# Kernel optimization log

Hardware: AMD Instinct MI355X
Metric: run time of the kernel (lower is better)

Reference implementation:

```python
import jax, jax.numpy as jnp
import numpy as np

B, L, D = 4, 1024, 512
H, DK = 8, 64
NL = 4
M_REL = 7
NEG = jnp.float32(-2**32 + 1)


def _layernorm(x, g, b, eps=1e-5):
    mu = jnp.mean(x, axis=-1, keepdims=True)
    var = jnp.var(x, axis=-1, keepdims=True)
    return (x - mu) * jax.lax.rsqrt(var + eps) * g + b


def setup_inputs() -> dict:
    key = jax.random.key(0)
    ks = jax.random.split(key, 24)
    s = 0.02
    inp = {
        "x": jax.random.normal(ks[0], (B, L, D), jnp.float32),
        "maskPAD": jnp.ones((B, L, L), jnp.int32),
        "WQ": jax.random.normal(ks[1], (NL, D, H * DK), jnp.float32) * s,
        "bQ": jnp.zeros((NL, H * DK), jnp.float32),
        "WK": jax.random.normal(ks[2], (NL, D, H * DK), jnp.float32) * s,
        "bK": jnp.zeros((NL, H * DK), jnp.float32),
        "WV": jax.random.normal(ks[3], (NL, D, H * DK), jnp.float32) * s,
        "bV": jnp.zeros((NL, H * DK), jnp.float32),
        "WO": jax.random.normal(ks[4], (NL, H * DK, D), jnp.float32) * s,
        "bO": jnp.zeros((NL, D), jnp.float32),
        "embK": jax.random.normal(ks[5], (NL, 2 * M_REL + 1, H), jnp.float32) * s + 1.0,
        "embB": jax.random.normal(ks[6], (NL, 2 * M_REL + 1, H), jnp.float32) * s,
        "ln1_g": jnp.ones((NL, D), jnp.float32),
        "ln1_b": jnp.zeros((NL, D), jnp.float32),
        "ln2_g": jnp.ones((NL, D), jnp.float32),
        "ln2_b": jnp.zeros((NL, D), jnp.float32),
        "Wf1": jax.random.normal(ks[7], (NL, D, 4 * D), jnp.float32) * s,
        "bf1": jnp.zeros((NL, 4 * D), jnp.float32),
        "Wf2": jax.random.normal(ks[8], (NL, 4 * D, D), jnp.float32) * s,
        "bf2": jnp.zeros((NL, D), jnp.float32),
    }
    return inp


def _rel_idx():
    # posIdx is None -> arange-based relative distance with log-bucketing beyond M_REL
    pos = jnp.arange(L, dtype=jnp.float32)
    d = jnp.abs(pos[:, None] - pos[None, :])  # [L, L]
    d = jnp.where(d > M_REL, M_REL + jnp.log2(jnp.maximum(d - M_REL, 1.0)), d)
    return jnp.clip(d, 0, 2 * M_REL).astype(jnp.int32)  # [L, L]


def reference(x, maskPAD, WQ, bQ, WK, bK, WV, bV, WO, bO, embK, embB,
              ln1_g, ln1_b, ln2_g, ln2_b, Wf1, bf1, Wf2, bf2):
    idx = _rel_idx()  # [L, L]
    mask0 = (maskPAD == 0)[:, None, :, :]  # [B, 1, L, L]
    scale = 1.0 / np.sqrt(DK)

    qx = kx = vx = x
    pre = None
    for i in range(NL):
        q = (qx @ WQ[i] + bQ[i]).reshape(B, L, H, DK).transpose(0, 2, 1, 3)
        k = (kx @ WK[i] + bK[i]).reshape(B, L, H, DK).transpose(0, 2, 1, 3)
        v = (vx @ WV[i] + bV[i]).reshape(B, L, H, DK).transpose(0, 2, 1, 3)
        scores = jnp.einsum('bhqd,bhkd->bhqk', q, k) * scale  # [B,H,L,L]
        # multiplicative + additive relative-position bias
        kb = embK[i][idx].transpose(2, 0, 1)  # [H, L, L]
        bb = embB[i][idx].transpose(2, 0, 1)
        scores = scores * kb[None] + bb[None]
        if pre is not None:
            scores = scores + pre  # Realformer residual score carry
        scores = jnp.where(mask0, NEG, scores)
        alpha = jax.nn.softmax(scores, axis=-1)
        z = jnp.einsum('bhqk,bhkd->bhqd', alpha, v)
        z = z.transpose(0, 2, 1, 3).reshape(B, L, H * DK) @ WO[i] + bO[i]
        # FFN (Realformer: residual around vx)
        h = _layernorm(vx + z, ln1_g[i], ln1_b[i])
        ffn = jax.nn.gelu(h @ Wf1[i] + bf1[i], approximate=False) @ Wf2[i] + bf2[i]
        xo = _layernorm(h + ffn, ln2_g[i], ln2_b[i])
        qx = kx = vx = xo
        pre = scores
    return xo
```

## Files before the change

### kernel.cpp

```cpp
#include <hip/hip_runtime.h>
#include <stdint.h>

typedef unsigned short u16;
typedef short bf16x8_t __attribute__((ext_vector_type(8)));
typedef float f32x4_t __attribute__((ext_vector_type(4)));
typedef u16 u16x8_t __attribute__((ext_vector_type(8)));

#define MFMA16(a,b,c) __builtin_amdgcn_mfma_f32_16x16x32_bf16((a),(b),(c),0,0,0)

__device__ __forceinline__ u16 f2bf(float f) {
  uint32_t u = __float_as_uint(f);
  u += 0x7fffu + ((u >> 16) & 1u);
  return (u16)(u >> 16);
}
__device__ __forceinline__ float bf2f(u16 h) {
  return __uint_as_float(((uint32_t)h) << 16);
}
__device__ __forceinline__ void gload16(const void* g, void* l) {
  __builtin_amdgcn_global_load_lds(
      (__attribute__((address_space(1))) void*)const_cast<void*>(g),
      (__attribute__((address_space(3))) void*)l, 16, 0, 0);
}

__global__ __launch_bounds__(256) void cvt_bf16(const float* __restrict__ in,
                                                u16* __restrict__ out, int n4) {
  int i = blockIdx.x * 256 + threadIdx.x;
  if (i >= n4) return;
  float4 v = ((const float4*)in)[i];
  ushort4 o;
  o.x = f2bf(v.x); o.y = f2bf(v.y); o.z = f2bf(v.z); o.w = f2bf(v.w);
  ((ushort4*)out)[i] = o;
}

__global__ __launch_bounds__(256) void mask2plane(const int* __restrict__ mask,
                                                  u16* __restrict__ mp, int n8) {
  int i = blockIdx.x * 256 + threadIdx.x;
  if (i >= n8) return;
  int4 a = ((const int4*)mask)[i * 2], b = ((const int4*)mask)[i * 2 + 1];
  u16x8_t o;
  o[0] = a.x == 0 ? 0xCF80 : 0; o[1] = a.y == 0 ? 0xCF80 : 0;
  o[2] = a.z == 0 ? 0xCF80 : 0; o[3] = a.w == 0 ? 0xCF80 : 0;
  o[4] = b.x == 0 ? 0xCF80 : 0; o[5] = b.y == 0 ? 0xCF80 : 0;
  o[6] = b.z == 0 ? 0xCF80 : 0; o[7] = b.w == 0 ? 0xCF80 : 0;
  ((u16x8_t*)mp)[i] = o;
}

__global__ __launch_bounds__(256) void transpose_w(
    const float* __restrict__ in, u16* __restrict__ out, int K, int N,
    size_t in_bstride, size_t out_bstride, size_t out_off) {
  __shared__ float tile[32][33];
  int p = blockIdx.z;
  const float* ip = in + (size_t)p * in_bstride;
  u16* op = out + (size_t)p * out_bstride + out_off;
  int n0 = blockIdx.x * 32, k0 = blockIdx.y * 32;
  int tx = threadIdx.x & 31, ty = threadIdx.x >> 5;
#pragma unroll
  for (int r = 0; r < 4; r++) {
    int k = ty + r * 8;
    tile[k][tx] = ip[(size_t)(k0 + k) * N + n0 + tx];
  }
  __syncthreads();
#pragma unroll
  for (int r = 0; r < 4; r++) {
    int n = ty + r * 8;
    op[(size_t)(n0 + n) * K + k0 + tx] = f2bf(tile[tx][n]);
  }
}

__global__ __launch_bounds__(256) void ln_kernel(
    const float* __restrict__ in, const float* __restrict__ g,
    const float* __restrict__ bb, float* __restrict__ outf,
    u16* __restrict__ outb) {
  int row = blockIdx.x * 4 + (threadIdx.x >> 6);
  int lane = threadIdx.x & 63;
  const float4* ip = (const float4*)(in + (size_t)row * 512);
  float4 a = ip[lane * 2], c = ip[lane * 2 + 1];
  float s = a.x + a.y + a.z + a.w + c.x + c.y + c.z + c.w;
  float q = a.x * a.x + a.y * a.y + a.z * a.z + a.w * a.w +
            c.x * c.x + c.y * c.y + c.z * c.z + c.w * c.w;
#pragma unroll
  for (int m = 1; m < 64; m <<= 1) {
    s += __shfl_xor(s, m);
    q += __shfl_xor(q, m);
  }
  float mean = s * (1.0f / 512.0f);
  float var = q * (1.0f / 512.0f) - mean * mean;
  float rstd = rsqrtf(var + 1e-5f);
  const float4* gp = (const float4*)g;
  const float4* bp = (const float4*)bb;
  float4 g1 = gp[lane * 2], g2 = gp[lane * 2 + 1];
  float4 b1 = bp[lane * 2], b2 = bp[lane * 2 + 1];
  float4 y1, y2;
  y1.x = (a.x - mean) * rstd * g1.x + b1.x;
  y1.y = (a.y - mean) * rstd * g1.y + b1.y;
  y1.z = (a.z - mean) * rstd * g1.z + b1.z;
  y1.w = (a.w - mean) * rstd * g1.w + b1.w;
  y2.x = (c.x - mean) * rstd * g2.x + b2.x;
  y2.y = (c.y - mean) * rstd * g2.y + b2.y;
  y2.z = (c.z - mean) * rstd * g2.z + b2.z;
  y2.w = (c.w - mean) * rstd * g2.w + b2.w;
  ((float4*)(outf + (size_t)row * 512))[lane * 2] = y1;
  ((float4*)(outf + (size_t)row * 512))[lane * 2 + 1] = y2;
  ushort4 u1, u2;
  u1.x = f2bf(y1.x); u1.y = f2bf(y1.y); u1.z = f2bf(y1.z); u1.w = f2bf(y1.w);
  u2.x = f2bf(y2.x); u2.y = f2bf(y2.y); u2.z = f2bf(y2.z); u2.w = f2bf(y2.w);
  ((ushort4*)(outb + (size_t)row * 512))[lane * 2] = u1;
  ((ushort4*)(outb + (size_t)row * 512))[lane * 2 + 1] = u2;
}

template <int BM, int BN, int EPI>
__global__ __launch_bounds__(256) void gemmT(
    const u16* __restrict__ A, const u16* __restrict__ Bt, int K, int N,
    const float* __restrict__ f0, const float* __restrict__ f1,
    const float* __restrict__ f2, u16* __restrict__ o0, u16* __restrict__ o1,
    u16* __restrict__ o2, float* __restrict__ of) {
  constexpr int MFR = BM / 32, NFR = BN / 32;
  __shared__ u16 As[BM * 64];
  __shared__ u16 Bs[BN * 64];
  int t = threadIdx.x, lane = t & 63, w = t >> 6;
  int wr = w >> 1, wc = w & 1, lg = lane >> 4, li = lane & 15;
  int bn = blockIdx.x, bm = blockIdx.y;
  const u16* Ab = A + (size_t)bm * BM * K;
  const u16* Bb = Bt + (size_t)bn * BN * K;
  f32x4_t acc[MFR][NFR] = {};
  for (int k0 = 0; k0 < K; k0 += 64) {
    if (k0) __syncthreads();
#pragma unroll
    for (int i = 0; i < BM / 32; i++) {
      int o = i * 256 + t, r = o >> 3, c = o & 7, cs = c ^ (r & 7);
      gload16(Ab + (size_t)r * K + k0 + cs * 8, As + (i * 256 + (t & ~63)) * 8);
    }
#pragma unroll
    for (int i = 0; i < BN / 32; i++) {
      int o = i * 256 + t, r = o >> 3, c = o & 7, cs = c ^ (r & 7);
      gload16(Bb + (size_t)r * K + k0 + cs * 8, Bs + (i * 256 + (t & ~63)) * 8);
    }
    __syncthreads();
#pragma unroll
    for (int kk = 0; kk < 2; kk++) {
      bf16x8_t af[MFR], bfv[NFR];
#pragma unroll
      for (int m = 0; m < MFR; m++) {
        int r = wr * (BM / 2) + m * 16 + li;
        int cb = (kk * 4 + lg) ^ (r & 7);
        af[m] = *(const bf16x8_t*)(As + r * 64 + cb * 8);
      }
#pragma unroll
      for (int n = 0; n < NFR; n++) {
        int r = wc * (BN / 2) + n * 16 + li;
        int cb = (kk * 4 + lg) ^ (r & 7);
        bfv[n] = *(const bf16x8_t*)(Bs + r * 64 + cb * 8);
      }
#pragma unroll
      for (int m = 0; m < MFR; m++)
#pragma unroll
        for (int n = 0; n < NFR; n++)
          acc[m][n] = MFMA16(af[m], bfv[n], acc[m][n]);
    }
  }
#pragma unroll
  for (int m = 0; m < MFR; m++) {
#pragma unroll
    for (int n = 0; n < NFR; n++) {
      int col = bn * BN + wc * (BN / 2) + n * 16 + li;
#pragma unroll
      for (int j = 0; j < 4; j++) {
        int row = bm * BM + wr * (BM / 2) + m * 16 + lg * 4 + j;
        float v = acc[m][n][j];
        if constexpr (EPI == 0) {
          int which = col >> 9, hd = col & 511, hh = hd >> 6, dk = hd & 63;
          const float* bp = which == 0 ? f0 : (which == 1 ? f1 : f2);
          float val = v + bp[hd];
          int b2 = row >> 10, l = row & 1023;
          if (which == 0)
            o0[(((size_t)(b2 * 8 + hh)) * 1024 + l) * 64 + dk] = f2bf(val);
          else if (which == 1)
            o1[(((size_t)(b2 * 8 + hh)) * 1024 + l) * 64 + dk] = f2bf(val);
          else
            o2[(((size_t)(b2 * 8 + hh)) * 64 + dk) * 1024 + l] = f2bf(val);
        } else if constexpr (EPI == 1 || EPI == 3) {
          float val = v + f0[col] + f1[(size_t)row * 512 + col];
          of[(size_t)row * N + col] = val;
        } else {
          float x = v + f0[col];
          float val = 0.5f * x * (1.0f + erff(x * 0.70710678118f));
          o0[(size_t)row * N + col] = f2bf(val);
        }
      }
    }
  }
}

template <int WPRE>
__global__ __launch_bounds__(512, 4) void attn_kernel(
    const u16* __restrict__ qb, const u16* __restrict__ kb,
    const u16* __restrict__ vb, u16* __restrict__ zout,
    const u16* __restrict__ preR, u16* __restrict__ preW, int firstLayer,
    const float* __restrict__ embK, const float* __restrict__ embB) {
  __shared__ u16 Ks[2][64 * 64];
  __shared__ u16 Vs[2][64 * 64];
  __shared__ u16 Pre[8][16 * 64];
  __shared__ float2 lutKB[1024];
  int t = threadIdx.x, lane = t & 63, w = t >> 6;
  int half = w >> 2, wl = w & 3, lg = lane >> 4, li = lane & 15;
  int tl = t & 255;
  int bh = blockIdx.y, b = bh >> 3, h = bh & 7;
  int q0 = blockIdx.x * 64;
  for (int d = t; d < 1024; d += 512) {
    int idx = (d <= 7) ? d : min(14, 38 - __clz(d - 7));
    lutKB[d] = make_float2(embK[idx * 8 + h] * 0.125f, embB[idx * 8 + h]);
  }
  float fK = embK[14 * 8 + h] * 0.125f, fB = embB[14 * 8 + h];
  const u16* qrow = qb + ((size_t)bh * 1024 + q0 + wl * 16 + li) * 64;
  bf16x8_t qf[2];
  qf[0] = *(const bf16x8_t*)(qrow + lg * 8);
  qf[1] = *(const bf16x8_t*)(qrow + 32 + lg * 8);
  float lrow[4] = {0.f, 0.f, 0.f, 0.f};
  f32x4_t oacc[4] = {};
  const u16* kbase = kb + (size_t)bh * 65536;
  const u16* vbase = vb + (size_t)bh * 65536;
  const u16* prb = firstLayer ? preR + (size_t)b * 1048576
                              : preR + (size_t)bh * 1048576;
  u16* pwb = preW + (size_t)bh * 1048576;
  u16* prw = (u16*)Pre[w];
  int qrow0 = q0 + wl * 16;
  for (int kt = 0; kt < 8; ++kt) {
    if (kt) __syncthreads();
    int k0 = half * 512 + kt * 64;
#pragma unroll
    for (int i = 0; i < 2; i++) {
      int o = i * 256 + tl, r = o >> 3, c = o & 7, cs = c ^ (r & 7);
      gload16(kbase + (size_t)(k0 + r) * 64 + cs * 8,
              Ks[half] + (i * 256 + (tl & ~63)) * 8);
      gload16(vbase + (size_t)r * 1024 + k0 + cs * 8,
              Vs[half] + (i * 256 + (tl & ~63)) * 8);
    }
#pragma unroll
    for (int i = 0; i < 2; i++) {
      int g = i * 64 + lane, r = g >> 3, c = g & 7, cs = c ^ (r & 7);
      gload16(prb + (size_t)(qrow0 + r) * 1024 + k0 + cs * 8, prw + g * 8);
    }
    __syncthreads();
    f32x4_t s[4] = {};
    __builtin_amdgcn_s_setprio(1);
#pragma unroll
    for (int kk = 0; kk < 2; kk++) {
#pragma unroll
      for (int n = 0; n < 4; n++) {
        int r = n * 16 + li;
        int cb = (kk * 4 + lg) ^ (r & 7);
        bf16x8_t kf = *(const bf16x8_t*)(Ks[half] + r * 64 + cb * 8);
        s[n] = MFMA16(qf[kk], kf, s[n]);
      }
    }
    __builtin_amdgcn_s_setprio(0);
    float sv[4][4];
    bool farTile = (k0 - (qrow0 + 15) >= 135) || (qrow0 - (k0 + 63) >= 135);
    if (farTile) {
#pragma unroll
      for (int n = 0; n < 4; n++) {
#pragma unroll
        for (int j = 0; j < 4; j++) {
          int row = lg * 4 + j, col = n * 16 + li;
          int pidx = (row * 64 + col) ^ ((row & 7) << 3);
          float val = fmaf(s[n][j], fK, fB) + bf2f(prw[pidx]);
          prw[pidx] = f2bf(val);
          sv[n][j] = val;
        }
      }
    } else {
      int dbase = qrow0 + lg * 4 - k0 - li;
#pragma unroll
      for (int n = 0; n < 4; n++) {
#pragma unroll
        for (int j = 0; j < 4; j++) {
          int d = abs(dbase + j - n * 16);
          int row = lg * 4 + j, col = n * 16 + li;
          int pidx = (row * 64 + col) ^ ((row & 7) << 3);
          float2 kb2 = lutKB[d];
          float val = fmaf(s[n][j], kb2.x, kb2.y) + bf2f(prw[pidx]);
          prw[pidx] = f2bf(val);
          sv[n][j] = val;
        }
      }
    }
    if (WPRE) {
#pragma unroll
      for (int i = 0; i < 2; i++) {
        int g = i * 64 + lane, r = g >> 3, c = g & 7, cs = c ^ (r & 7);
        *(u16x8_t*)(pwb + (size_t)(qrow0 + r) * 1024 + k0 + cs * 8) =
            *(const u16x8_t*)(prw + g * 8);
      }
    }
#pragma unroll
    for (int n = 0; n < 4; n++) {
#pragma unroll
      for (int j = 0; j < 4; j++) {
        float p = __expf(sv[n][j]);
        lrow[j] += p;
        int row = lg * 4 + j, col = n * 16 + li;
        prw[(row * 64 + col) ^ ((row & 7) << 3)] = f2bf(p);
      }
    }
    __builtin_amdgcn_s_setprio(1);
#pragma unroll
    for (int kk = 0; kk < 2; kk++) {
      int cbp = (kk * 4 + lg) ^ (li & 7);
      bf16x8_t pf = *(const bf16x8_t*)(prw + li * 64 + cbp * 8);
#pragma unroll
      for (int n = 0; n < 4; n++) {
        int r = n * 16 + li;
        int cb = (kk * 4 + lg) ^ (r & 7);
        bf16x8_t vf = *(const bf16x8_t*)(Vs[half] + r * 64 + cb * 8);
        oacc[n] = MFMA16(pf, vf, oacc[n]);
      }
    }
    __builtin_amdgcn_s_setprio(0);
  }
#pragma unroll
  for (int j = 0; j < 4; j++)
#pragma unroll
    for (int m2 = 1; m2 < 16; m2 <<= 1) lrow[j] += __shfl_xor(lrow[j], m2);
  __syncthreads();
  float* Om = (float*)Ks;
  float* Ml = (float*)Vs;
  if (half == 1) {
#pragma unroll
    for (int n = 0; n < 4; n++)
#pragma unroll
      for (int j = 0; j < 4; j++)
        Om[(wl * 16 + lg * 4 + j) * 64 + n * 16 + li] = oacc[n][j];
    if (li == 0)
#pragma unroll
      for (int j = 0; j < 4; j++) Ml[wl * 16 + lg * 4 + j] = lrow[j];
  }
  __syncthreads();
  if (half == 0) {
#pragma unroll
    for (int j = 0; j < 4; j++) {
      int row = wl * 16 + lg * 4 + j;
      float inv = 1.0f / (lrow[j] + Ml[row]);
      int qq = q0 + row;
#pragma unroll
      for (int n = 0; n < 4; n++) {
        zout[((size_t)b * 1024 + qq) * 512 + h * 64 + n * 16 + li] =
            f2bf((oacc[n][j] + Om[row * 64 + n * 16 + li]) * inv);
      }
    }
  }
}

extern "C" void kernel_launch(void* const* d_in, const int* in_sizes, int n_in,
                              void* d_out, int out_size, void* d_ws,
                              size_t ws_size, hipStream_t stream) {
  const float* x = (const float*)d_in[0];
  const int* maskPAD = (const int*)d_in[1];
  const float* WQ = (const float*)d_in[2];
  const float* bQ = (const float*)d_in[3];
  const float* WK = (const float*)d_in[4];
  const float* bK = (const float*)d_in[5];
  const float* WV = (const float*)d_in[6];
  const float* bV = (const float*)d_in[7];
  const float* WO = (const float*)d_in[8];
  const float* bO = (const float*)d_in[9];
  const float* embK = (const float*)d_in[10];
  const float* embB = (const float*)d_in[11];
  const float* ln1g = (const float*)d_in[12];
  const float* ln1b = (const float*)d_in[13];
  const float* ln2g = (const float*)d_in[14];
  const float* ln2b = (const float*)d_in[15];
  const float* Wf1 = (const float*)d_in[16];
  const float* bf1 = (const float*)d_in[17];
  const float* Wf2 = (const float*)d_in[18];
  const float* bf2 = (const float*)d_in[19];

  char* ws = (char*)d_ws;
  u16* pre = (u16*)(ws + 0);
  u16* qkvw = (u16*)(ws + 67108864);
  u16* wot = (u16*)(ws + 73400320);
  u16* wf1t = (u16*)(ws + 75497472);
  u16* wf2t = (u16*)(ws + 83886080);
  u16* xb = (u16*)(ws + 92274688);
  u16* qbuf = (u16*)(ws + 96468992);
  u16* kbuf = (u16*)(ws + 100663296);
  u16* vbuf = (u16*)(ws + 104857600);
  u16* zg = (u16*)(ws + 109051904);
  float* tbuf = (float*)(ws + 125829120);
  float* hbuf = (float*)(ws + 134217728);
  float* vxbuf = (float*)(ws + 142606336);
  u16* mp = (u16*)vxbuf;

  dim3 tb(256);
  mask2plane<<<2048, tb, 0, stream>>>(maskPAD, mp, 524288);
  cvt_bf16<<<2048, tb, 0, stream>>>(x, xb, 524288);
  transpose_w<<<dim3(16, 16, 4), tb, 0, stream>>>(WQ, qkvw, 512, 512,
                                                  512 * 512, 1536 * 512, 0);
  transpose_w<<<dim3(16, 16, 4), tb, 0, stream>>>(WK, qkvw, 512, 512,
                                                  512 * 512, 1536 * 512, 262144);
  transpose_w<<<dim3(16, 16, 4), tb, 0, stream>>>(WV, qkvw, 512, 512,
                                                  512 * 512, 1536 * 512, 524288);
  transpose_w<<<dim3(16, 16, 4), tb, 0, stream>>>(WO, wot, 512, 512, 512 * 512,
                                                  512 * 512, 0);
  transpose_w<<<dim3(64, 16, 4), tb, 0, stream>>>(Wf1, wf1t, 512, 2048,
                                                  512 * 2048, 2048 * 512, 0);
  transpose_w<<<dim3(16, 64, 4), tb, 0, stream>>>(Wf2, wf2t, 2048, 512,
                                                  2048 * 512, 512 * 2048, 0);

  for (int i = 0; i < 4; i++) {
    gemmT<64, 128, 0><<<dim3(12, 64), tb, 0, stream>>>(
        xb, qkvw + (size_t)i * 1536 * 512, 512, 1536, bQ + i * 512,
        bK + i * 512, bV + i * 512, qbuf, kbuf, vbuf, nullptr);
    if (i < 3)
      attn_kernel<1><<<dim3(16, 32), dim3(512), 0, stream>>>(
          qbuf, kbuf, vbuf, zg, (i == 0 ? mp : pre), pre, (i == 0 ? 1 : 0),
          embK + i * 120, embB + i * 120);
    else
      attn_kernel<0><<<dim3(16, 32), dim3(512), 0, stream>>>(
          qbuf, kbuf, vbuf, zg, pre, pre, 0, embK + i * 120, embB + i * 120);
    gemmT<64, 64, 1><<<dim3(8, 64), tb, 0, stream>>>(
        zg, wot + (size_t)i * 512 * 512, 512, 512, bO + i * 512,
        (i == 0 ? x : vxbuf), nullptr, nullptr, nullptr, nullptr, tbuf);
    ln_kernel<<<1024, tb, 0, stream>>>(tbuf, ln1g + i * 512, ln1b + i * 512,
                                       hbuf, xb);
    gemmT<64, 128, 2><<<dim3(16, 64), tb, 0, stream>>>(
        xb, wf1t + (size_t)i * 2048 * 512, 512, 2048, bf1 + i * 2048, nullptr,
        nullptr, zg, nullptr, nullptr, nullptr);
    gemmT<64, 64, 3><<<dim3(8, 64), tb, 0, stream>>>(
        zg, wf2t + (size_t)i * 512 * 2048, 2048, 512, bf2 + i * 512, hbuf,
        nullptr, nullptr, nullptr, nullptr, tbuf);
    ln_kernel<<<1024, tb, 0, stream>>>(tbuf, ln2g + i * 512, ln2b + i * 512,
                                       (i == 3 ? (float*)d_out : vxbuf), xb);
  }
}
```

Baseline: 624.2 us.

## Store score-residual carry in MFMA fragment order and prefetch it into registers

The residual score carry (pre) and the initial mask plane now use a fragment-major layout that matches the MFMA accumulator ownership. Each lane can then load and store its 16 values with two 16-byte vector accesses directly from registers instead of staging through LDS. The next tile's carry is prefetched into registers during the current tile, and the exp/row-sum is fused into the bias loop. Barriers become explicit s_barrier calls with waitcnt, and the LDS use for the LUT and merge buffers shrinks. The intermediate pre buffer layout is now private to these kernels, and it adds register pressure.

Result: faster. 605.6 us (-3.0%).

```diff
diff --git a/kernel.cpp b/kernel.cpp
--- a/kernel.cpp
+++ b/kernel.cpp
@@ -32,17 +32,30 @@
   ((ushort4*)out)[i] = o;
 }
 
-__global__ __launch_bounds__(256) void mask2plane(const int* __restrict__ mask,
-                                                  u16* __restrict__ mp, int n8) {
-  int i = blockIdx.x * 256 + threadIdx.x;
-  if (i >= n8) return;
-  int4 a = ((const int4*)mask)[i * 2], b = ((const int4*)mask)[i * 2 + 1];
-  u16x8_t o;
-  o[0] = a.x == 0 ? 0xCF80 : 0; o[1] = a.y == 0 ? 0xCF80 : 0;
-  o[2] = a.z == 0 ? 0xCF80 : 0; o[3] = a.w == 0 ? 0xCF80 : 0;
-  o[4] = b.x == 0 ? 0xCF80 : 0; o[5] = b.y == 0 ? 0xCF80 : 0;
-  o[6] = b.z == 0 ? 0xCF80 : 0; o[7] = b.w == 0 ? 0xCF80 : 0;
-  ((u16x8_t*)mp)[i] = o;
+__global__ __launch_bounds__(256) void mask2planeF(const int* __restrict__ mask,
+                                                   u16* __restrict__ mpF) {
+  int blk = blockIdx.x;
+  int kt = blk & 7, half = (blk >> 3) & 1, qblk = (blk >> 4) & 15, b = blk >> 8;
+  int wl = threadIdx.x >> 6, lane = threadIdx.x & 63;
+  int lg = lane >> 4, li = lane & 15;
+  int q0 = qblk * 64 + wl * 16 + lg * 4;
+  int k0 = (half * 8 + kt) * 64 + li;
+  const int* mb = mask + (size_t)b * 1048576;
+  u16x8_t c0, c1;
+#pragma unroll
+  for (int n = 0; n < 4; n++) {
+#pragma unroll
+    for (int j = 0; j < 4; j++) {
+      u16 v = (mb[(size_t)(q0 + j) * 1024 + k0 + n * 16] == 0) ? (u16)0xCF80
+                                                               : (u16)0;
+      if (n < 2) c0[n * 4 + j] = v;
+      else c1[(n - 2) * 4 + j] = v;
+    }
+  }
+  size_t off = ((((size_t)(b * 16 + qblk) * 2 + half) * 8 + kt) * 4 + wl) * 1024 +
+               (size_t)lane * 16;
+  *(u16x8_t*)(mpF + off) = c0;
+  *(u16x8_t*)(mpF + off + 8) = c1;
 }
 
 __global__ __launch_bounds__(256) void transpose_w(
@@ -199,18 +212,21 @@
     const float* __restrict__ embK, const float* __restrict__ embB) {
   __shared__ u16 Ks[2][64 * 64];
   __shared__ u16 Vs[2][64 * 64];
-  __shared__ u16 Pre[8][16 * 64];
-  __shared__ float2 lutKB[1024];
+  __shared__ u16 Ps[8][16 * 64];
+  __shared__ float2 lutKB[256];
+  __shared__ float Ml[64];
   int t = threadIdx.x, lane = t & 63, w = t >> 6;
   int half = w >> 2, wl = w & 3, lg = lane >> 4, li = lane & 15;
   int tl = t & 255;
   int bh = blockIdx.y, b = bh >> 3, h = bh & 7;
-  int q0 = blockIdx.x * 64;
-  for (int d = t; d < 1024; d += 512) {
+  int qblk = blockIdx.x;
+  int q0 = qblk * 64;
+  if (t < 256) {
+    int d = t;
     int idx = (d <= 7) ? d : min(14, 38 - __clz(d - 7));
     lutKB[d] = make_float2(embK[idx * 8 + h] * 0.125f, embB[idx * 8 + h]);
   }
-  float fK = embK[14 * 8 + h] * 0.125f, fB = embB[14 * 8 + h];
+  float fK = embK[112 + h] * 0.125f, fB = embB[112 + h];
   const u16* qrow = qb + ((size_t)bh * 1024 + q0 + wl * 16 + li) * 64;
   bf16x8_t qf[2];
   qf[0] = *(const bf16x8_t*)(qrow + lg * 8);
@@ -222,10 +238,14 @@
   const u16* prb = firstLayer ? preR + (size_t)b * 1048576
                               : preR + (size_t)bh * 1048576;
   u16* pwb = preW + (size_t)bh * 1048576;
-  u16* prw = (u16*)Pre[w];
+  u16* prw = (u16*)Ps[w];
   int qrow0 = q0 + wl * 16;
+  size_t pbase =
+      ((((size_t)(qblk * 2 + half) * 8) * 4 + wl) * 64 + lane) * 16;
+  u16x8_t pA = *(const u16x8_t*)(prb + pbase);
+  u16x8_t pB = *(const u16x8_t*)(prb + pbase + 8);
+  u16x8_t nA = {}, nB = {};
   for (int kt = 0; kt < 8; ++kt) {
-    if (kt) __syncthreads();
     int k0 = half * 512 + kt * 64;
 #pragma unroll
     for (int i = 0; i < 2; i++) {
@@ -235,12 +255,14 @@
       gload16(vbase + (size_t)r * 1024 + k0 + cs * 8,
               Vs[half] + (i * 256 + (tl & ~63)) * 8);
     }
-#pragma unroll
-    for (int i = 0; i < 2; i++) {
-      int g = i * 64 + lane, r = g >> 3, c = g & 7, cs = c ^ (r & 7);
-      gload16(prb + (size_t)(qrow0 + r) * 1024 + k0 + cs * 8, prw + g * 8);
-    }
-    __syncthreads();
+    asm volatile("s_waitcnt vmcnt(0) lgkmcnt(0)" ::: "memory");
+    __builtin_amdgcn_s_barrier();
+    __builtin_amdgcn_sched_barrier(0);
+    if (kt < 7) {
+      size_t np = pbase + (size_t)(kt + 1) * 4096;
+      nA = *(const u16x8_t*)(prb + np);
+      nB = *(const u16x8_t*)(prb + np + 8);
+    }
     f32x4_t s[4] = {};
     __builtin_amdgcn_s_setprio(1);
 #pragma unroll
@@ -254,18 +276,21 @@
       }
     }
     __builtin_amdgcn_s_setprio(0);
-    float sv[4][4];
+    u16x8_t oA, oB;
     bool farTile = (k0 - (qrow0 + 15) >= 135) || (qrow0 - (k0 + 63) >= 135);
     if (farTile) {
 #pragma unroll
       for (int n = 0; n < 4; n++) {
 #pragma unroll
         for (int j = 0; j < 4; j++) {
+          float pv = bf2f(n < 2 ? pA[n * 4 + j] : pB[(n - 2) * 4 + j]);
+          float val = fmaf(s[n][j], fK, fB) + pv;
+          u16 vb16 = f2bf(val);
+          if (n < 2) oA[n * 4 + j] = vb16; else oB[(n - 2) * 4 + j] = vb16;
+          float p = __expf(val);
+          lrow[j] += p;
           int row = lg * 4 + j, col = n * 16 + li;
-          int pidx = (row * 64 + col) ^ ((row & 7) << 3);
-          float val = fmaf(s[n][j], fK, fB) + bf2f(prw[pidx]);
-          prw[pidx] = f2bf(val);
-          sv[n][j] = val;
+          prw[(row * 64 + col) ^ ((row & 7) << 3)] = f2bf(p);
         }
       }
     } else {
@@ -275,32 +300,22 @@
 #pragma unroll
         for (int j = 0; j < 4; j++) {
           int d = abs(dbase + j - n * 16);
+          float2 kb2 = lutKB[d];
+          float pv = bf2f(n < 2 ? pA[n * 4 + j] : pB[(n - 2) * 4 + j]);
+          float val = fmaf(s[n][j], kb2.x, kb2.y) + pv;
+          u16 vb16 = f2bf(val);
+          if (n < 2) oA[n * 4 + j] = vb16; else oB[(n - 2) * 4 + j] = vb16;
+          float p = __expf(val);
+          lrow[j] += p;
           int row = lg * 4 + j, col = n * 16 + li;
-          int pidx = (row * 64 + col) ^ ((row & 7) << 3);
-          float2 kb2 = lutKB[d];
-          float val = fmaf(s[n][j], kb2.x, kb2.y) + bf2f(prw[pidx]);
-          prw[pidx] = f2bf(val);
-          sv[n][j] = val;
+          prw[(row * 64 + col) ^ ((row & 7) << 3)] = f2bf(p);
         }
       }
     }
     if (WPRE) {
-#pragma unroll
-      for (int i = 0; i < 2; i++) {
-        int g = i * 64 + lane, r = g >> 3, c = g & 7, cs = c ^ (r & 7);
-        *(u16x8_t*)(pwb + (size_t)(qrow0 + r) * 1024 + k0 + cs * 8) =
-            *(const u16x8_t*)(prw + g * 8);
-      }
-    }
-#pragma unroll
-    for (int n = 0; n < 4; n++) {
-#pragma unroll
-      for (int j = 0; j < 4; j++) {
-        float p = __expf(sv[n][j]);
-        lrow[j] += p;
-        int row = lg * 4 + j, col = n * 16 + li;
-        prw[(row * 64 + col) ^ ((row & 7) << 3)] = f2bf(p);
-      }
+      size_t po = pbase + (size_t)kt * 4096;
+      *(u16x8_t*)(pwb + po) = oA;
+      *(u16x8_t*)(pwb + po + 8) = oB;
     }
     __builtin_amdgcn_s_setprio(1);
 #pragma unroll
@@ -316,14 +331,20 @@
       }
     }
     __builtin_amdgcn_s_setprio(0);
+    __builtin_amdgcn_sched_barrier(0);
+    __builtin_amdgcn_s_barrier();
+    __builtin_amdgcn_sched_barrier(0);
+    pA = nA;
+    pB = nB;
   }
 #pragma unroll
   for (int j = 0; j < 4; j++)
 #pragma unroll
     for (int m2 = 1; m2 < 16; m2 <<= 1) lrow[j] += __shfl_xor(lrow[j], m2);
-  __syncthreads();
-  float* Om = (float*)Ks;
-  float* Ml = (float*)Vs;
+  asm volatile("s_waitcnt vmcnt(0) lgkmcnt(0)" ::: "memory");
+  __builtin_amdgcn_s_barrier();
+  __builtin_amdgcn_sched_barrier(0);
+  float* Om = (float*)Ps;
   if (half == 1) {
 #pragma unroll
     for (int n = 0; n < 4; n++)
@@ -334,7 +355,9 @@
 #pragma unroll
       for (int j = 0; j < 4; j++) Ml[wl * 16 + lg * 4 + j] = lrow[j];
   }
-  __syncthreads();
+  asm volatile("s_waitcnt vmcnt(0) lgkmcnt(0)" ::: "memory");
+  __builtin_amdgcn_s_barrier();
+  __builtin_amdgcn_sched_barrier(0);
   if (half == 0) {
 #pragma unroll
     for (int j = 0; j < 4; j++) {
@@ -388,10 +411,10 @@
   float* tbuf = (float*)(ws + 125829120);
   float* hbuf = (float*)(ws + 134217728);
   float* vxbuf = (float*)(ws + 142606336);
-  u16* mp = (u16*)vxbuf;
+  u16* mpF = (u16*)vxbuf;
 
   dim3 tb(256);
-  mask2plane<<<2048, tb, 0, stream>>>(maskPAD, mp, 524288);
+  mask2planeF<<<1024, tb, 0, stream>>>(maskPAD, mpF);
   cvt_bf16<<<2048, tb, 0, stream>>>(x, xb, 524288);
   transpose_w<<<dim3(16, 16, 4), tb, 0, stream>>>(WQ, qkvw, 512, 512,
                                                   512 * 512, 1536 * 512, 0);
@@ -412,7 +435,7 @@
         bK + i * 512, bV + i * 512, qbuf, kbuf, vbuf, nullptr);
     if (i < 3)
       attn_kernel<1><<<dim3(16, 32), dim3(512), 0, stream>>>(
-          qbuf, kbuf, vbuf, zg, (i == 0 ? mp : pre), pre, (i == 0 ? 1 : 0),
+          qbuf, kbuf, vbuf, zg, (i == 0 ? mpF : pre), pre, (i == 0 ? 1 : 0),
           embK + i * 120, embB + i * 120);
     else
       attn_kernel<0><<<dim3(16, 32), dim3(512), 0, stream>>>(
```
